# Optimization experiments

Hardware: AMD Instinct MI355X
Metric: run time of the kernel (lower is better)

Reference implementation:

```python
import jax, jax.numpy as jnp
import numpy as np

N = 50000; E = 800000; H = 4; C = 64; FEAT = 128; EDIM = 16; G = 256
NEG_SLOPE = 0.2; BN_EPS = 1e-5


def _gat_layer(x, src, dst, W, a_src, a_dst, bias, gamma, beta, alpha_edge=None):
    # GATConv (concat=True, PyG math), then BatchNorm1d (batch stats) + ReLU.
    h = (x @ W).reshape(N, H, C)                       # [N,H,C]
    alpha = (h * a_src).sum(-1)[src] + (h * a_dst).sum(-1)[dst]   # [Etot,H]
    if alpha_edge is not None:
        alpha = alpha + alpha_edge
    alpha = jax.nn.leaky_relu(alpha, NEG_SLOPE)
    amax = jax.ops.segment_max(alpha, dst, num_segments=N)        # edge softmax over dst
    ea = jnp.exp(alpha - amax[dst])
    denom = jax.ops.segment_sum(ea, dst, num_segments=N)
    coef = ea / (denom[dst] + 1e-16)
    out = jax.ops.segment_sum(coef[:, :, None] * h[src], dst, num_segments=N)
    out = out.reshape(N, H * C) + bias
    mu = out.mean(0)
    var = out.var(0)
    out = (out - mu) / jnp.sqrt(var + BN_EPS) * gamma + beta
    return jax.nn.relu(out)


def setup_inputs() -> dict:
    key = jax.random.key(0)
    ks = jax.random.split(key, 32)
    s = 0.05
    inp = {
        "x": jax.random.normal(ks[0], (N, FEAT), jnp.float32),
        "edge_index": jax.random.randint(ks[1], (2, E), 0, N),
        "edge_attr": jax.random.normal(ks[2], (E, EDIM), jnp.float32),
        "batch": jnp.sort(jax.random.randint(ks[3], (N,), 0, G)),
    }
    in_dims = [FEAT, H * C, H * C]
    for i in range(3):
        k = 4 + 7 * i
        inp[f"W{i}"] = jax.random.normal(ks[k], (in_dims[i], H * C), jnp.float32) * s
        inp[f"att_src{i}"] = jax.random.normal(ks[k + 1], (H, C), jnp.float32) * s
        inp[f"att_dst{i}"] = jax.random.normal(ks[k + 2], (H, C), jnp.float32) * s
        inp[f"bias{i}"] = jnp.zeros((H * C,), jnp.float32)
        inp[f"gamma{i}"] = jnp.ones((H * C,), jnp.float32)
        inp[f"beta{i}"] = jnp.zeros((H * C,), jnp.float32)
    inp["We0"] = jax.random.normal(ks[28], (EDIM, H * C), jnp.float32) * s
    inp["att_e0"] = jax.random.normal(ks[29], (H, C), jnp.float32) * s
    return inp


def reference(x, edge_index, edge_attr, batch,
              W0, att_src0, att_dst0, bias0, gamma0, beta0,
              W1, att_src1, att_dst1, bias1, gamma1, beta1,
              W2, att_src2, att_dst2, bias2, gamma2, beta2,
              We0, att_e0):
    # PyG GATConv adds self-loops; edge_attr for self-loops filled with mean.
    loops = jnp.arange(N)
    src = jnp.concatenate([edge_index[0], loops])
    dst = jnp.concatenate([edge_index[1], loops])
    ea_sl = jnp.concatenate([edge_attr, jnp.broadcast_to(edge_attr.mean(0), (N, EDIM))], 0)
    e = (ea_sl @ We0).reshape(E + N, H, C)
    alpha_e = (e * att_e0).sum(-1)                     # [Etot,H]
    x = _gat_layer(x, src, dst, W0, att_src0, att_dst0, bias0, gamma0, beta0, alpha_e)
    x = _gat_layer(x, src, dst, W1, att_src1, att_dst1, bias1, gamma1, beta1)
    x = _gat_layer(x, src, dst, W2, att_src2, att_dst2, bias2, gamma2, beta2)
    # global_mean_pool
    counts = jax.ops.segment_sum(jnp.ones((N,), x.dtype), batch, num_segments=G)
    sums = jax.ops.segment_sum(x, batch, num_segments=G)
    return sums / jnp.clip(counts, 1.0)[:, None]
```

## Files before the change

### kernel.cpp

```cpp
#include <hip/hip_runtime.h>
#include <math.h>

#define NN 50000
#define NE 800000
#define ET 850000
#define HCC 256
#define GG 256
#define CAP 64
#define NB 16

constexpr int RTILES = 782;

constexpr size_t NHC    = (size_t)NN * HCC;
constexpr size_t O_H    = 0;
constexpr size_t O_AGG  = O_H + NHC / 2;
constexpr size_t O_REC  = O_AGG + NHC / 2;
constexpr size_t O_BT0  = O_REC + (size_t)NN * CAP * 4;
constexpr size_t O_BT1  = O_BT0 + 16384;
constexpr size_t O_BT2  = O_BT1 + 32768;
constexpr size_t O_AS   = O_BT2 + 32768;
constexpr size_t O_AD   = O_AS + (size_t)NN * 4;
constexpr size_t O_M    = O_AD + (size_t)NN * 4;
constexpr size_t O_ZERO = O_M + 64;
constexpr size_t O_DEG  = O_ZERO;
constexpr size_t O_SLS  = O_DEG + NN;
constexpr size_t O_PART = O_SLS + 4;
constexpr size_t O_END  = O_PART + 3 * NB * 512;
constexpr size_t ZWORDS = O_END - O_ZERO;
constexpr int    ZBLK   = (int)((ZWORDS / 4 + 255) / 256);
constexpr int    XBLK   = (int)((size_t)NN * 128 / 2048);

typedef __attribute__((ext_vector_type(8))) short bf16x8;
typedef __attribute__((ext_vector_type(4))) float f32x4;

__device__ inline unsigned short f2bf(float f) {
    unsigned int u = __float_as_uint(f);
    unsigned int r = (u + 0x7fffu + ((u >> 16) & 1u)) >> 16;
    return (unsigned short)r;
}
__device__ inline float b2f(unsigned short u) {
    return __uint_as_float(((unsigned int)u) << 16);
}
__device__ inline float bflo(unsigned int u) { return __uint_as_float(u << 16); }
__device__ inline float bfhi(unsigned int u) { return __uint_as_float(u & 0xffff0000u); }

__global__ void prep_kernel(const float* __restrict__ W0, const float* __restrict__ W1,
                            const float* __restrict__ W2,
                            const float* __restrict__ We0, const float* __restrict__ att_e0,
                            unsigned short* __restrict__ Bt0,
                            unsigned short* __restrict__ Bt1,
                            unsigned short* __restrict__ Bt2,
                            float* __restrict__ M, float* __restrict__ zbase,
                            const float* __restrict__ x, unsigned short* __restrict__ xb) {
    int b = blockIdx.x;
    if (b >= 641 + ZBLK) {
        size_t i0 = ((size_t)(b - (641 + ZBLK)) * 256 + threadIdx.x) * 8;
        float4 f1 = *(const float4*)(x + i0);
        float4 f2 = *(const float4*)(x + i0 + 4);
        uint4 o;
        o.x = ((unsigned)f2bf(f1.y) << 16) | f2bf(f1.x);
        o.y = ((unsigned)f2bf(f1.w) << 16) | f2bf(f1.z);
        o.z = ((unsigned)f2bf(f2.y) << 16) | f2bf(f2.x);
        o.w = ((unsigned)f2bf(f2.w) << 16) | f2bf(f2.z);
        *(uint4*)(xb + i0) = o;
        return;
    }
    if (b >= 641) {
        size_t idx = ((size_t)(b - 641) * 256 + threadIdx.x) * 4;
        if (idx < ZWORDS)
            *(float4*)(zbase + idx) = make_float4(0.f, 0.f, 0.f, 0.f);
        return;
    }
    if (b == 640) {
        int t = threadIdx.x;
        if (t < 64) {
            int k = t >> 2, hh = t & 3;
            float s = 0.f;
            for (int c = 0; c < 64; ++c)
                s += We0[k * 256 + hh * 64 + c] * att_e0[hh * 64 + c];
            M[k * 4 + hh] = s;
        }
        return;
    }
    const float* W; unsigned short* Bt; int K, base;
    if (b < 128)      { W = W0; Bt = Bt0; K = 128; base = 0; }
    else if (b < 384) { W = W1; Bt = Bt1; K = 256; base = 128; }
    else              { W = W2; Bt = Bt2; K = 256; base = 384; }
    int idx = (b - base) * 256 + threadIdx.x;
    int n = idx & 255, k = idx >> 8;
    Bt[(size_t)n * K + k] = f2bf(W[(size_t)k * 256 + n]);
}

__global__ void csr_kernel(const int* __restrict__ srcA, const int* __restrict__ dstA,
                           const float* __restrict__ ea, const float* __restrict__ M,
                           int* __restrict__ deg, uint4* __restrict__ rec,
                           float* __restrict__ slsum) {
    int t0 = blockIdx.x * 2048 + threadIdx.x;
    float a0 = 0.f, a1 = 0.f, a2 = 0.f, a3 = 0.f;
    #pragma unroll
    for (int q = 0; q < 8; ++q) {
        int e = t0 + q * 256;
        if (e < ET) {
            bool real = (e < NE);
            int d = real ? dstA[e] : (e - NE);
            int s = real ? srcA[e] : (e - NE);
            int p = atomicAdd(&deg[d], 1);
            if (p > CAP - 1) p = CAP - 1;
            int slot = d * CAP + p;
            uint4 r;
            r.z = (unsigned)s;
            if (real) {
                r.w = 0u;
                const float4* pp = (const float4*)(ea + (size_t)e * 16);
                float4 va = pp[0], vb = pp[1], vc = pp[2], vd = pp[3];
                float v[16] = {va.x, va.y, va.z, va.w, vb.x, vb.y, vb.z, vb.w,
                               vc.x, vc.y, vc.z, vc.w, vd.x, vd.y, vd.z, vd.w};
                float o0 = 0.f, o1 = 0.f, o2 = 0.f, o3 = 0.f;
                #pragma unroll
                for (int k = 0; k < 16; ++k) {
                    float4 m4 = *(const float4*)(M + k * 4);
                    o0 = fmaf(v[k], m4.x, o0);
                    o1 = fmaf(v[k], m4.y, o1);
                    o2 = fmaf(v[k], m4.z, o2);
                    o3 = fmaf(v[k], m4.w, o3);
                }
                r.x = ((unsigned)f2bf(o1) << 16) | (unsigned)f2bf(o0);
                r.y = ((unsigned)f2bf(o3) << 16) | (unsigned)f2bf(o2);
                a0 += o0; a1 += o1; a2 += o2; a3 += o3;
            } else {
                r.x = 0u; r.y = 0u; r.w = 1u;
            }
            rec[slot] = r;
        }
    }
    #pragma unroll
    for (int off = 32; off; off >>= 1) {
        a0 += __shfl_xor(a0, off);
        a1 += __shfl_xor(a1, off);
        a2 += __shfl_xor(a2, off);
        a3 += __shfl_xor(a3, off);
    }
    __shared__ float part[4][4];
    int wave = threadIdx.x >> 6, lane = threadIdx.x & 63;
    if (lane == 0) {
        part[wave][0] = a0; part[wave][1] = a1;
        part[wave][2] = a2; part[wave][3] = a3;
    }
    __syncthreads();
    if (threadIdx.x < 4)
        atomicAdd(&slsum[threadIdx.x],
                  part[0][threadIdx.x] + part[1][threadIdx.x] +
                  part[2][threadIdx.x] + part[3][threadIdx.x]);
}

template <int K, bool NORM>
__global__ __launch_bounds__(512) void gemm2(const unsigned short* __restrict__ Ab,
                                             const unsigned short* __restrict__ Bt,
                                             const float* __restrict__ part,
                                             const float* __restrict__ gamma,
                                             const float* __restrict__ beta,
                                             const float* __restrict__ att_src,
                                             const float* __restrict__ att_dst,
                                             unsigned short* __restrict__ Hout,
                                             float* __restrict__ asA,
                                             float* __restrict__ adA, int M) {
    constexpr int KP  = K + 8;
    constexpr int NLD = K / 64;
    __shared__ unsigned short Bs[128][KP];
    __shared__ unsigned short As[2][64][KP];
    __shared__ float kvs[256], cvs[256];

    int tid = threadIdx.x;
    int wave = tid >> 6, lane = tid & 63;
    int quad = lane >> 4, l16 = lane & 15;
    int wr = wave >> 1, wc = wave & 1;

    int b = blockIdx.x;
    int cb = (b >> 3) & 1;
    int ts = ((b >> 4) << 3) | (b & 7);
    int np = (int)(gridDim.x >> 1);
    int colbase = cb * 128;
    int head = cb * 2 + wc;

    if (NORM) {
        if (tid < 256) {
            int ch = tid;
            float s = 0.f, s2 = 0.f;
            #pragma unroll
            for (int q = 0; q < NB; ++q) {
                s  += part[q * 512 + ch];
                s2 += part[q * 512 + 256 + ch];
            }
            const float invN = 1.0f / (float)NN;
            float mr = s * invN;
            float var = s2 * invN - mr * mr;
            float k = gamma[ch] * rsqrtf(var + 1e-5f);
            kvs[ch] = k;
            cvs[ch] = beta[ch] - mr * k;
        }
    }
    {
        constexpr int TOT = 128 * K;
        for (int idx = tid * 8; idx < TOT; idx += 4096) {
            int br = idx / K, bk = idx % K;
            uint4 v = *(const uint4*)(Bt + (size_t)(colbase + br) * K + bk);
            *(uint4*)&Bs[br][bk] = v;
        }
    }

    int srow = tid >> 3;
    const int scol0 = (tid & 7) * (K / 8);

    uint4 ldA_[NLD], ldB_[NLD];

    auto issue = [&](uint4 (&ld)[NLD], int t) {
        int r = t * 64 + srow;
        if (r < M) {
            const uint4* src = (const uint4*)(Ab + (size_t)r * K + scol0);
            #pragma unroll
            for (int q = 0; q < NLD; ++q) ld[q] = src[q];
        } else {
            #pragma unroll
            for (int q = 0; q < NLD; ++q) ld[q] = make_uint4(0u, 0u, 0u, 0u);
        }
    };
    auto commit = [&](uint4 (&ld)[NLD], int buf) {
        #pragma unroll
        for (int q = 0; q < NLD; ++q) {
            uint4 v = ld[q];
            if (NORM) {
                int ch = scol0 + q * 8;
                float u[8] = {bflo(v.x), bfhi(v.x), bflo(v.y), bfhi(v.y),
                              bflo(v.z), bfhi(v.z), bflo(v.w), bfhi(v.w)};
                #pragma unroll
                for (int j = 0; j < 8; ++j)
                    u[j] = fmaxf(fmaf(u[j], kvs[ch + j], cvs[ch + j]), 0.f);
                v.x = ((unsigned)f2bf(u[1]) << 16) | f2bf(u[0]);
                v.y = ((unsigned)f2bf(u[3]) << 16) | f2bf(u[2]);
                v.z = ((unsigned)f2bf(u[5]) << 16) | f2bf(u[4]);
                v.w = ((unsigned)f2bf(u[7]) << 16) | f2bf(u[6]);
            }
            *(uint4*)&As[buf][srow][scol0 + q * 8] = v;
        }
    };

    float asc[4], adc_[4];
    #pragma unroll
    for (int ni = 0; ni < 4; ++ni) {
        int c = colbase + wc * 64 + ni * 16 + l16;
        asc[ni]  = att_src[c];
        adc_[ni] = att_dst[c];
    }

    __syncthreads();

    auto tilestep = [&](uint4 (&ldCur)[NLD], uint4 (&ldNxt)[NLD], int buf, int t, int tn) {
        if (tn < RTILES) issue(ldNxt, tn);
        commit(ldCur, buf);
        __syncthreads();
        f32x4 acc[4] = {};
        #pragma unroll
        for (int k0 = 0; k0 < K; k0 += 32) {
            bf16x8 af, bfr[4];
            af = *(const bf16x8*)&As[buf][wr * 16 + l16][k0 + quad * 8];
            #pragma unroll
            for (int ni = 0; ni < 4; ++ni)
                bfr[ni] = *(const bf16x8*)&Bs[wc * 64 + ni * 16 + l16][k0 + quad * 8];
            #pragma unroll
            for (int ni = 0; ni < 4; ++ni)
                acc[ni] = __builtin_amdgcn_mfma_f32_16x16x32_bf16(
                    af, bfr[ni], acc[ni], 0, 0, 0);
        }
        int row0 = t * 64 + wr * 16;
        #pragma unroll
        for (int reg = 0; reg < 4; ++reg) {
            int r = row0 + quad * 4 + reg;
            if (r < M) {
                #pragma unroll
                for (int ni = 0; ni < 4; ++ni) {
                    int c = colbase + wc * 64 + ni * 16 + l16;
                    Hout[(size_t)r * HCC + c] = f2bf(acc[ni][reg]);
                }
            }
            float s1 = acc[0][reg] * asc[0] + acc[1][reg] * asc[1] +
                       acc[2][reg] * asc[2] + acc[3][reg] * asc[3];
            float d1 = acc[0][reg] * adc_[0] + acc[1][reg] * adc_[1] +
                       acc[2][reg] * adc_[2] + acc[3][reg] * adc_[3];
            #pragma unroll
            for (int off = 1; off < 16; off <<= 1) {
                s1 += __shfl_xor(s1, off);
                d1 += __shfl_xor(d1, off);
            }
            if (l16 == 0 && r < M) {
                asA[(size_t)r * 4 + head] = s1;
                adA[(size_t)r * 4 + head] = d1;
            }
        }
    };

    int t = ts;
    issue(ldA_, t);
    while (t < RTILES) {
        int t1 = t + np;
        tilestep(ldA_, ldB_, 0, t, t1);
        t = t1;
        if (t >= RTILES) break;
        int t2 = t + np;
        tilestep(ldB_, ldA_, 1, t, t2);
        t = t2;
    }
}

template <bool HAS_AE>
__global__ __launch_bounds__(512) void agg_kernel(const unsigned short* __restrict__ Hm,
                                                  const float* __restrict__ asA,
                                                  const float* __restrict__ adA,
                                                  const uint4* __restrict__ rec,
                                                  const int* __restrict__ degA,
                                                  const float* __restrict__ slsum,
                                                  unsigned short* __restrict__ outA,
                                                  float* __restrict__ part) {
    __shared__ float wlds[8][260];
    __shared__ float slds[2][8][256];
    int wave = threadIdx.x >> 6, lane = threadIdx.x & 63;
    int n = blockIdx.x * 8 + wave;
    int head = lane >> 4;
    int st = n * CAP;
    int d = degA[n];
    if (d > CAP) d = CAP;
    float4 ad4 = *(const float4*)(adA + (size_t)n * 4);

    float4 w4 = make_float4(0.f, 0.f, 0.f, 0.f);
    int ms = 0;
    if (lane < d) {
        uint4 r = rec[st + lane];
        ms = (int)r.z;
        float4 av = *(const float4*)(asA + (size_t)ms * 4);
        float4 t = make_float4(av.x + ad4.x, av.y + ad4.y, av.z + ad4.z, av.w + ad4.w);
        if (HAS_AE) {
            if (r.w) {
                const float inv = 1.0f / (float)NE;
                t.x += slsum[0] * inv; t.y += slsum[1] * inv;
                t.z += slsum[2] * inv; t.w += slsum[3] * inv;
            } else {
                t.x += bflo(r.x); t.y += bfhi(r.x);
                t.z += bflo(r.y); t.w += bfhi(r.y);
            }
        }
        t.x = (t.x > 0.f) ? t.x : 0.2f * t.x;
        t.y = (t.y > 0.f) ? t.y : 0.2f * t.y;
        t.z = (t.z > 0.f) ? t.z : 0.2f * t.z;
        t.w = (t.w > 0.f) ? t.w : 0.2f * t.w;
        w4.x = __expf(t.x);
        w4.y = __expf(t.y);
        w4.z = __expf(t.z);
        w4.w = __expf(t.w);
    }
    float4 Dv = w4;
    wlds[wave][0 * 65 + lane] = w4.x;
    wlds[wave][1 * 65 + lane] = w4.y;
    wlds[wave][2 * 65 + lane] = w4.z;
    wlds[wave][3 * 65 + lane] = w4.w;

    float4 acc = make_float4(0.f, 0.f, 0.f, 0.f);
    const unsigned short* hb = Hm + lane * 4;
    int cnt8 = (d + 7) & ~7;
    const float* wrow = &wlds[wave][head * 65];

    int sjA[8]; ushort4 hvA[8];
    #pragma unroll
    for (int q = 0; q < 8; ++q)
        sjA[q] = __builtin_amdgcn_readlane(ms, q);
    #pragma unroll
    for (int q = 0; q < 8; ++q)
        hvA[q] = *(const ushort4*)(hb + (size_t)sjA[q] * HCC);
    for (int jj = 0; jj < cnt8; jj += 8) {
        int nj = jj + 8;
        bool more = (nj < cnt8);
        ushort4 hvB[8];
        if (more) {
            int sjB[8];
            #pragma unroll
            for (int q = 0; q < 8; ++q)
                sjB[q] = __builtin_amdgcn_readlane(ms, nj + q);
            #pragma unroll
            for (int q = 0; q < 8; ++q)
                hvB[q] = *(const ushort4*)(hb + (size_t)sjB[q] * HCC);
        }
        float wq[8];
        #pragma unroll
        for (int q = 0; q < 8; ++q)
            wq[q] = wrow[jj + q];
        #pragma unroll
        for (int q = 0; q < 8; ++q) {
            acc.x = fmaf(wq[q], b2f(hvA[q].x), acc.x);
            acc.y = fmaf(wq[q], b2f(hvA[q].y), acc.y);
            acc.z = fmaf(wq[q], b2f(hvA[q].z), acc.z);
            acc.w = fmaf(wq[q], b2f(hvA[q].w), acc.w);
        }
        if (more) {
            #pragma unroll
            for (int q = 0; q < 8; ++q)
                hvA[q] = hvB[q];
        }
    }
    #pragma unroll
    for (int off = 32; off; off >>= 1) {
        Dv.x += __shfl_xor(Dv.x, off);
        Dv.y += __shfl_xor(Dv.y, off);
        Dv.z += __shfl_xor(Dv.z, off);
        Dv.w += __shfl_xor(Dv.w, off);
    }
    float D = (head & 2) ? ((head & 1) ? Dv.w : Dv.z) : ((head & 1) ? Dv.y : Dv.x);
    float inv = 1.0f / (D + 1e-16f);
    float4 o = make_float4(acc.x * inv, acc.y * inv, acc.z * inv, acc.w * inv);
    ushort4 ob = make_ushort4(f2bf(o.x), f2bf(o.y), f2bf(o.z), f2bf(o.w));
    *(ushort4*)(outA + (size_t)n * HCC + lane * 4) = ob;

    *(float4*)&slds[0][wave][lane * 4] = o;
    *(float4*)&slds[1][wave][lane * 4] =
        make_float4(o.x * o.x, o.y * o.y, o.z * o.z, o.w * o.w);
    __syncthreads();
    int t = threadIdx.x;
    if (t < 512) {
        int ch = t & 255, which = t >> 8;
        float s = 0.f;
        #pragma unroll
        for (int w = 0; w < 8; ++w)
            s += slds[which][w][ch];
        int bucket = blockIdx.x & (NB - 1);
        atomicAdd(&part[bucket * 512 + which * 256 + ch], s);
    }
}

__global__ void pool_kernel(const unsigned short* __restrict__ aggb,
                            const float* __restrict__ part,
                            const float* __restrict__ gamma, const float* __restrict__ beta,
                            const int* __restrict__ batch,
                            float* __restrict__ out) {
    int ch = threadIdx.x;
    int g = blockIdx.x;
    float s = 0.f, s2 = 0.f;
    #pragma unroll
    for (int b = 0; b < NB; ++b) {
        s  += part[b * 512 + ch];
        s2 += part[b * 512 + 256 + ch];
    }
    const float invN = 1.0f / (float)NN;
    float mr = s * invN;
    float var = s2 * invN - mr * mr;
    float k = gamma[ch] * rsqrtf(var + 1e-5f);
    float c = beta[ch] - mr * k;

    int lo = 0, hi = NN;
    while (lo < hi) { int mid = (lo + hi) >> 1; if (batch[mid] < g) lo = mid + 1; else hi = mid; }
    int start = lo;
    lo = start; hi = NN;
    while (lo < hi) { int mid = (lo + hi) >> 1; if (batch[mid] < g + 1) lo = mid + 1; else hi = mid; }
    int end = lo;

    float a0 = 0.f, a1 = 0.f, a2 = 0.f, a3 = 0.f;
    int n = start;
    for (; n + 3 < end; n += 4) {
        a0 += fmaxf(fmaf(b2f(aggb[(size_t)n * HCC + ch]), k, c), 0.f);
        a1 += fmaxf(fmaf(b2f(aggb[(size_t)(n + 1) * HCC + ch]), k, c), 0.f);
        a2 += fmaxf(fmaf(b2f(aggb[(size_t)(n + 2) * HCC + ch]), k, c), 0.f);
        a3 += fmaxf(fmaf(b2f(aggb[(size_t)(n + 3) * HCC + ch]), k, c), 0.f);
    }
    for (; n < end; ++n)
        a0 += fmaxf(fmaf(b2f(aggb[(size_t)n * HCC + ch]), k, c), 0.f);
    float tot = (a0 + a1) + (a2 + a3);
    out[(size_t)g * HCC + ch] = tot / fmaxf((float)(end - start), 1.0f);
}

extern "C" void kernel_launch(void* const* d_in, const int* in_sizes, int n_in,
                              void* d_out, int out_size, void* d_ws, size_t ws_size,
                              hipStream_t stream) {
    const float* x = (const float*)d_in[0];
    const int* edge_index = (const int*)d_in[1];
    const int* srcA = edge_index;
    const int* dstA = edge_index + NE;
    const float* edge_attr = (const float*)d_in[2];
    const int* batch = (const int*)d_in[3];
    const float* W[3]   = {(const float*)d_in[4],  (const float*)d_in[10], (const float*)d_in[16]};
    const float* asc[3] = {(const float*)d_in[5],  (const float*)d_in[11], (const float*)d_in[17]};
    const float* adc[3] = {(const float*)d_in[6],  (const float*)d_in[12], (const float*)d_in[18]};
    const float* gam[3] = {(const float*)d_in[8],  (const float*)d_in[14], (const float*)d_in[20]};
    const float* bet[3] = {(const float*)d_in[9],  (const float*)d_in[15], (const float*)d_in[21]};
    const float* We0 = (const float*)d_in[22];
    const float* att_e0 = (const float*)d_in[23];

    float* wsf = (float*)d_ws;
    unsigned short* hbuf = (unsigned short*)(wsf + O_H);
    unsigned short* aggb = (unsigned short*)(wsf + O_AGG);
    unsigned short* xb   = aggb;
    uint4* rec   = (uint4*)(wsf + O_REC);
    unsigned short* Bt0  = (unsigned short*)(wsf + O_BT0);
    unsigned short* Bt1  = (unsigned short*)(wsf + O_BT1);
    unsigned short* Bt2  = (unsigned short*)(wsf + O_BT2);
    float* asA   = wsf + O_AS;
    float* adA   = wsf + O_AD;
    float* Mb    = wsf + O_M;
    int*   deg   = (int*)(wsf + O_DEG);
    float* slsum = wsf + O_SLS;
    float* part  = wsf + O_PART;

    prep_kernel<<<641 + ZBLK + XBLK, 256, 0, stream>>>(W[0], W[1], W[2], We0, att_e0,
                                                       Bt0, Bt1, Bt2, Mb, wsf + O_ZERO,
                                                       x, xb);
    csr_kernel<<<(ET + 2047) / 2048, 256, 0, stream>>>(srcA, dstA, edge_attr, Mb,
                                                       deg, rec, slsum);

    gemm2<128, false><<<512, 512, 0, stream>>>(xb, Bt0, (const float*)0,
        (const float*)0, (const float*)0, asc[0], adc[0], hbuf, asA, adA, NN);
    agg_kernel<true><<<6250, 512, 0, stream>>>(hbuf, asA, adA, rec, deg, slsum,
        aggb, part + (size_t)0 * NB * 512);

    gemm2<256, true><<<256, 512, 0, stream>>>(aggb, Bt1, part + (size_t)0 * NB * 512,
        gam[0], bet[0], asc[1], adc[1], hbuf, asA, adA, NN);
    agg_kernel<false><<<6250, 512, 0, stream>>>(hbuf, asA, adA, rec, deg, slsum,
        aggb, part + (size_t)1 * NB * 512);

    gemm2<256, true><<<256, 512, 0, stream>>>(aggb, Bt2, part + (size_t)1 * NB * 512,
        gam[1], bet[1], asc[2], adc[2], hbuf, asA, adA, NN);
    agg_kernel<false><<<6250, 512, 0, stream>>>(hbuf, asA, adA, rec, deg, slsum,
        aggb, part + (size_t)2 * NB * 512);

    pool_kernel<<<GG, 256, 0, stream>>>(aggb, part + (size_t)2 * NB * 512,
                                        gam[2], bet[2], batch, (float*)d_out);
}
```

Before: 506.9 us.

## Load GEMM A fragments directly to registers, dropping LDS staging and double buffer

The node-feature GEMM kernel no longer stages A tiles through shared memory with a double-buffered pipeline and block barriers. Each wave now owns independent 16-row units and loads its A fragment directly from global memory into registers in MFMA layout, with BN+ReLU applied in registers. Launch bounds allow more blocks per CU, and layers 1-2 use twice as many blocks. This removes the LDS round-trip and per-tile barriers, but gives up cross-tile prefetch and relies on 50000 being divisible by 16, since row bounds checks are removed.

Result: slower. 744.4 us (+46.9%).

```diff
diff --git a/kernel.cpp b/kernel.cpp
--- a/kernel.cpp
+++ b/kernel.cpp
@@ -8,8 +8,6 @@
 #define GG 256
 #define CAP 64
 #define NB 16
-
-constexpr int RTILES = 782;
 
 constexpr size_t NHC    = (size_t)NN * HCC;
 constexpr size_t O_H    = 0;
@@ -154,33 +152,32 @@
 }
 
 template <int K, bool NORM>
-__global__ __launch_bounds__(512) void gemm2(const unsigned short* __restrict__ Ab,
-                                             const unsigned short* __restrict__ Bt,
-                                             const float* __restrict__ part,
-                                             const float* __restrict__ gamma,
-                                             const float* __restrict__ beta,
-                                             const float* __restrict__ att_src,
-                                             const float* __restrict__ att_dst,
-                                             unsigned short* __restrict__ Hout,
-                                             float* __restrict__ asA,
-                                             float* __restrict__ adA, int M) {
-    constexpr int KP  = K + 8;
-    constexpr int NLD = K / 64;
+__global__ __launch_bounds__(512, 4) void gemm3(const unsigned short* __restrict__ Ab,
+                                                const unsigned short* __restrict__ Bt,
+                                                const float* __restrict__ part,
+                                                const float* __restrict__ gamma,
+                                                const float* __restrict__ beta,
+                                                const float* __restrict__ att_src,
+                                                const float* __restrict__ att_dst,
+                                                unsigned short* __restrict__ Hout,
+                                                float* __restrict__ asA,
+                                                float* __restrict__ adA) {
+    constexpr int KP = K + 8;
+    constexpr int NS = K / 32;
     __shared__ unsigned short Bs[128][KP];
-    __shared__ unsigned short As[2][64][KP];
     __shared__ float kvs[256], cvs[256];
 
     int tid = threadIdx.x;
     int wave = tid >> 6, lane = tid & 63;
     int quad = lane >> 4, l16 = lane & 15;
-    int wr = wave >> 1, wc = wave & 1;
+    int slot = wave >> 1, wc = wave & 1;
 
     int b = blockIdx.x;
     int cb = (b >> 3) & 1;
-    int ts = ((b >> 4) << 3) | (b & 7);
-    int np = (int)(gridDim.x >> 1);
+    int pair = ((b >> 4) << 3) | (b & 7);
     int colbase = cb * 128;
     int head = cb * 2 + wc;
+    int unit = pair * 4 + slot;
 
     if (NORM) {
         if (tid < 256) {
@@ -208,79 +205,64 @@
         }
     }
 
-    int srow = tid >> 3;
-    const int scol0 = (tid & 7) * (K / 8);
-
-    uint4 ldA_[NLD], ldB_[NLD];
-
-    auto issue = [&](uint4 (&ld)[NLD], int t) {
-        int r = t * 64 + srow;
-        if (r < M) {
-            const uint4* src = (const uint4*)(Ab + (size_t)r * K + scol0);
-            #pragma unroll
-            for (int q = 0; q < NLD; ++q) ld[q] = src[q];
-        } else {
-            #pragma unroll
-            for (int q = 0; q < NLD; ++q) ld[q] = make_uint4(0u, 0u, 0u, 0u);
-        }
-    };
-    auto commit = [&](uint4 (&ld)[NLD], int buf) {
+    float asc[4], adc_[4];
+    #pragma unroll
+    for (int ni = 0; ni < 4; ++ni) {
+        int c = colbase + wc * 64 + ni * 16 + l16;
+        asc[ni]  = att_src[c];
+        adc_[ni] = att_dst[c];
+    }
+
+    __syncthreads();
+
+    for (int t = unit; t < 3125; t += 1024) {
+        int row = t * 16 + l16;
+        const unsigned short* ap = Ab + (size_t)row * K + quad * 8;
+        uint4 al[NS];
         #pragma unroll
-        for (int q = 0; q < NLD; ++q) {
-            uint4 v = ld[q];
+        for (int s = 0; s < NS; ++s)
+            al[s] = *(const uint4*)(ap + s * 32);
+
+        f32x4 acc[4] = {};
+        #pragma unroll
+        for (int s = 0; s < NS; ++s) {
+            union { uint4 u; bf16x8 h; } cvt;
             if (NORM) {
-                int ch = scol0 + q * 8;
+                uint4 v = al[s];
+                int ch = s * 32 + quad * 8;
                 float u[8] = {bflo(v.x), bfhi(v.x), bflo(v.y), bfhi(v.y),
                               bflo(v.z), bfhi(v.z), bflo(v.w), bfhi(v.w)};
                 #pragma unroll
                 for (int j = 0; j < 8; ++j)
                     u[j] = fmaxf(fmaf(u[j], kvs[ch + j], cvs[ch + j]), 0.f);
-                v.x = ((unsigned)f2bf(u[1]) << 16) | f2bf(u[0]);
-                v.y = ((unsigned)f2bf(u[3]) << 16) | f2bf(u[2]);
-                v.z = ((unsigned)f2bf(u[5]) << 16) | f2bf(u[4]);
-                v.w = ((unsigned)f2bf(u[7]) << 16) | f2bf(u[6]);
-            }
-            *(uint4*)&As[buf][srow][scol0 + q * 8] = v;
-        }
-    };
-
-    float asc[4], adc_[4];
-    #pragma unroll
-    for (int ni = 0; ni < 4; ++ni) {
-        int c = colbase + wc * 64 + ni * 16 + l16;
-        asc[ni]  = att_src[c];
-        adc_[ni] = att_dst[c];
-    }
-
-    __syncthreads();
-
-    auto tilestep = [&](uint4 (&ldCur)[NLD], uint4 (&ldNxt)[NLD], int buf, int t, int tn) {
-        if (tn < RTILES) issue(ldNxt, tn);
-        commit(ldCur, buf);
-        __syncthreads();
-        f32x4 acc[4] = {};
-        #pragma unroll
-        for (int k0 = 0; k0 < K; k0 += 32) {
-            bf16x8 af, bfr[4];
-            af = *(const bf16x8*)&As[buf][wr * 16 + l16][k0 + quad * 8];
+                uint4 w;
+                w.x = ((unsigned)f2bf(u[1]) << 16) | f2bf(u[0]);
+                w.y = ((unsigned)f2bf(u[3]) << 16) | f2bf(u[2]);
+                w.z = ((unsigned)f2bf(u[5]) << 16) | f2bf(u[4]);
+                w.w = ((unsigned)f2bf(u[7]) << 16) | f2bf(u[6]);
+                cvt.u = w;
+            } else {
+                cvt.u = al[s];
+            }
+            bf16x8 af = cvt.h;
+            bf16x8 bfr[4];
             #pragma unroll
             for (int ni = 0; ni < 4; ++ni)
-                bfr[ni] = *(const bf16x8*)&Bs[wc * 64 + ni * 16 + l16][k0 + quad * 8];
+                bfr[ni] = *(const bf16x8*)&Bs[wc * 64 + ni * 16 + l16][s * 32 + quad * 8];
             #pragma unroll
             for (int ni = 0; ni < 4; ++ni)
                 acc[ni] = __builtin_amdgcn_mfma_f32_16x16x32_bf16(
                     af, bfr[ni], acc[ni], 0, 0, 0);
         }
-        int row0 = t * 64 + wr * 16;
+
+        int row0 = t * 16;
         #pragma unroll
         for (int reg = 0; reg < 4; ++reg) {
             int r = row0 + quad * 4 + reg;
-            if (r < M) {
-                #pragma unroll
-                for (int ni = 0; ni < 4; ++ni) {
-                    int c = colbase + wc * 64 + ni * 16 + l16;
-                    Hout[(size_t)r * HCC + c] = f2bf(acc[ni][reg]);
-                }
+            #pragma unroll
+            for (int ni = 0; ni < 4; ++ni) {
+                int c = colbase + wc * 64 + ni * 16 + l16;
+                Hout[(size_t)r * HCC + c] = f2bf(acc[ni][reg]);
             }
             float s1 = acc[0][reg] * asc[0] + acc[1][reg] * asc[1] +
                        acc[2][reg] * asc[2] + acc[3][reg] * asc[3];
@@ -291,23 +273,11 @@
                 s1 += __shfl_xor(s1, off);
                 d1 += __shfl_xor(d1, off);
             }
-            if (l16 == 0 && r < M) {
+            if (l16 == 0) {
                 asA[(size_t)r * 4 + head] = s1;
                 adA[(size_t)r * 4 + head] = d1;
             }
         }
-    };
-
-    int t = ts;
-    issue(ldA_, t);
-    while (t < RTILES) {
-        int t1 = t + np;
-        tilestep(ldA_, ldB_, 0, t, t1);
-        t = t1;
-        if (t >= RTILES) break;
-        int t2 = t + np;
-        tilestep(ldB_, ldA_, 1, t, t2);
-        t = t2;
     }
 }
 
@@ -511,18 +481,18 @@
     csr_kernel<<<(ET + 2047) / 2048, 256, 0, stream>>>(srcA, dstA, edge_attr, Mb,
                                                        deg, rec, slsum);
 
-    gemm2<128, false><<<512, 512, 0, stream>>>(xb, Bt0, (const float*)0,
-        (const float*)0, (const float*)0, asc[0], adc[0], hbuf, asA, adA, NN);
+    gemm3<128, false><<<512, 512, 0, stream>>>(xb, Bt0, (const float*)0,
+        (const float*)0, (const float*)0, asc[0], adc[0], hbuf, asA, adA);
     agg_kernel<true><<<6250, 512, 0, stream>>>(hbuf, asA, adA, rec, deg, slsum,
         aggb, part + (size_t)0 * NB * 512);
 
-    gemm2<256, true><<<256, 512, 0, stream>>>(aggb, Bt1, part + (size_t)0 * NB * 512,
-        gam[0], bet[0], asc[1], adc[1], hbuf, asA, adA, NN);
+    gemm3<256, true><<<512, 512, 0, stream>>>(aggb, Bt1, part + (size_t)0 * NB * 512,
+        gam[0], bet[0], asc[1], adc[1], hbuf, asA, adA);
     agg_kernel<false><<<6250, 512, 0, stream>>>(hbuf, asA, adA, rec, deg, slsum,
         aggb, part + (size_t)1 * NB * 512);
 
-    gemm2<256, true><<<256, 512, 0, stream>>>(aggb, Bt2, part + (size_t)1 * NB * 512,
-        gam[1], bet[1], asc[2], adc[2], hbuf, asA, adA, NN);
+    gemm3<256, true><<<512, 512, 0, stream>>>(aggb, Bt2, part + (size_t)1 * NB * 512,
+        gam[1], bet[1], asc[2], adc[2], hbuf, asA, adA);
     agg_kernel<false><<<6250, 512, 0, stream>>>(hbuf, asA, adA, rec, deg, slsum,
         aggb, part + (size_t)2 * NB * 512);
 
```

## Fuse layer-0 GEMM with CSR build and deepen aggregation gather prefetch

Applied to the files above, without the earlier changes.

Merges the CSR/edge-record construction and the first-layer GEMM into a single launch, with separate block ranges, so the two independent stages run concurrently and one launch gap disappears. The aggregation kernel now uses 256-thread blocks with 4 nodes each, doubling the block count. Its neighbor gather is restructured into two 8-wide register buffers, so two batches of loads are in flight instead of one. These changes raise register pressure in the aggregation kernel, and the fused kernel's CSR blocks share the GPU with GEMM blocks.

New measurement: 520.0 us. +2.6%, slower.

```diff
diff --git a/kernel.cpp b/kernel.cpp
--- a/kernel.cpp
+++ b/kernel.cpp
@@ -10,6 +10,8 @@
 #define NB 16
 
 constexpr int RTILES = 782;
+constexpr int G0B    = 512;
+constexpr int CSRB   = 416;
 
 constexpr size_t NHC    = (size_t)NN * HCC;
 constexpr size_t O_H    = 0;
@@ -91,66 +93,197 @@
     Bt[(size_t)n * K + k] = f2bf(W[(size_t)k * 256 + n]);
 }
 
-__global__ void csr_kernel(const int* __restrict__ srcA, const int* __restrict__ dstA,
-                           const float* __restrict__ ea, const float* __restrict__ M,
-                           int* __restrict__ deg, uint4* __restrict__ rec,
-                           float* __restrict__ slsum) {
-    int t0 = blockIdx.x * 2048 + threadIdx.x;
-    float a0 = 0.f, a1 = 0.f, a2 = 0.f, a3 = 0.f;
+__global__ __launch_bounds__(512) void g0csr(const unsigned short* __restrict__ Ab,
+                                             const unsigned short* __restrict__ Bt,
+                                             const float* __restrict__ att_src,
+                                             const float* __restrict__ att_dst,
+                                             unsigned short* __restrict__ Hout,
+                                             float* __restrict__ asA,
+                                             float* __restrict__ adA,
+                                             const int* __restrict__ srcA,
+                                             const int* __restrict__ dstA,
+                                             const float* __restrict__ ea,
+                                             const float* __restrict__ Mm,
+                                             int* __restrict__ deg,
+                                             uint4* __restrict__ rec,
+                                             float* __restrict__ slsum) {
+    constexpr int K   = 128;
+    constexpr int KP  = K + 8;
+    constexpr int NLD = K / 64;
+    __shared__ unsigned short Bs[128][KP];
+    __shared__ unsigned short As[2][64][KP];
+    __shared__ float prt[8][4];
+
+    int tid = threadIdx.x;
+    int wave = tid >> 6, lane = tid & 63;
+
+    if (blockIdx.x >= G0B) {
+        int t0 = (int)(blockIdx.x - G0B) * 2048 + tid;
+        float a0 = 0.f, a1 = 0.f, a2 = 0.f, a3 = 0.f;
+        #pragma unroll
+        for (int q = 0; q < 4; ++q) {
+            int e = t0 + q * 512;
+            if (e < ET) {
+                bool real = (e < NE);
+                int d = real ? dstA[e] : (e - NE);
+                int s = real ? srcA[e] : (e - NE);
+                int p = atomicAdd(&deg[d], 1);
+                if (p > CAP - 1) p = CAP - 1;
+                int slot = d * CAP + p;
+                uint4 r;
+                r.z = (unsigned)s;
+                if (real) {
+                    r.w = 0u;
+                    const float4* pp = (const float4*)(ea + (size_t)e * 16);
+                    float4 va = pp[0], vb = pp[1], vc = pp[2], vd = pp[3];
+                    float v[16] = {va.x, va.y, va.z, va.w, vb.x, vb.y, vb.z, vb.w,
+                                   vc.x, vc.y, vc.z, vc.w, vd.x, vd.y, vd.z, vd.w};
+                    float o0 = 0.f, o1 = 0.f, o2 = 0.f, o3 = 0.f;
+                    #pragma unroll
+                    for (int k = 0; k < 16; ++k) {
+                        float4 m4 = *(const float4*)(Mm + k * 4);
+                        o0 = fmaf(v[k], m4.x, o0);
+                        o1 = fmaf(v[k], m4.y, o1);
+                        o2 = fmaf(v[k], m4.z, o2);
+                        o3 = fmaf(v[k], m4.w, o3);
+                    }
+                    r.x = ((unsigned)f2bf(o1) << 16) | (unsigned)f2bf(o0);
+                    r.y = ((unsigned)f2bf(o3) << 16) | (unsigned)f2bf(o2);
+                    a0 += o0; a1 += o1; a2 += o2; a3 += o3;
+                } else {
+                    r.x = 0u; r.y = 0u; r.w = 1u;
+                }
+                rec[slot] = r;
+            }
+        }
+        #pragma unroll
+        for (int off = 32; off; off >>= 1) {
+            a0 += __shfl_xor(a0, off);
+            a1 += __shfl_xor(a1, off);
+            a2 += __shfl_xor(a2, off);
+            a3 += __shfl_xor(a3, off);
+        }
+        if (lane == 0) {
+            prt[wave][0] = a0; prt[wave][1] = a1;
+            prt[wave][2] = a2; prt[wave][3] = a3;
+        }
+        __syncthreads();
+        if (tid < 4) {
+            float s = 0.f;
+            #pragma unroll
+            for (int w = 0; w < 8; ++w) s += prt[w][tid];
+            atomicAdd(&slsum[tid], s);
+        }
+        return;
+    }
+
+    int quad = lane >> 4, l16 = lane & 15;
+    int wr = wave >> 1, wc = wave & 1;
+
+    int b = blockIdx.x;
+    int cb = (b >> 3) & 1;
+    int ts = ((b >> 4) << 3) | (b & 7);
+    const int np = G0B >> 1;
+    int colbase = cb * 128;
+    int head = cb * 2 + wc;
+
+    {
+        constexpr int TOT = 128 * K;
+        for (int idx = tid * 8; idx < TOT; idx += 4096) {
+            int br = idx / K, bk = idx % K;
+            uint4 v = *(const uint4*)(Bt + (size_t)(colbase + br) * K + bk);
+            *(uint4*)&Bs[br][bk] = v;
+        }
+    }
+
+    int srow = tid >> 3;
+    const int scol0 = (tid & 7) * (K / 8);
+
+    uint4 ldA_[NLD], ldB_[NLD];
+
+    auto issue = [&](uint4 (&ld)[NLD], int t) {
+        int r = t * 64 + srow;
+        if (r < NN) {
+            const uint4* src = (const uint4*)(Ab + (size_t)r * K + scol0);
+            #pragma unroll
+            for (int q = 0; q < NLD; ++q) ld[q] = src[q];
+        } else {
+            #pragma unroll
+            for (int q = 0; q < NLD; ++q) ld[q] = make_uint4(0u, 0u, 0u, 0u);
+        }
+    };
+    auto commit = [&](uint4 (&ld)[NLD], int buf) {
+        #pragma unroll
+        for (int q = 0; q < NLD; ++q)
+            *(uint4*)&As[buf][srow][scol0 + q * 8] = ld[q];
+    };
+
+    float asc[4], adc_[4];
     #pragma unroll
-    for (int q = 0; q < 8; ++q) {
-        int e = t0 + q * 256;
-        if (e < ET) {
-            bool real = (e < NE);
-            int d = real ? dstA[e] : (e - NE);
-            int s = real ? srcA[e] : (e - NE);
-            int p = atomicAdd(&deg[d], 1);
-            if (p > CAP - 1) p = CAP - 1;
-            int slot = d * CAP + p;
-            uint4 r;
-            r.z = (unsigned)s;
-            if (real) {
-                r.w = 0u;
-                const float4* pp = (const float4*)(ea + (size_t)e * 16);
-                float4 va = pp[0], vb = pp[1], vc = pp[2], vd = pp[3];
-                float v[16] = {va.x, va.y, va.z, va.w, vb.x, vb.y, vb.z, vb.w,
-                               vc.x, vc.y, vc.z, vc.w, vd.x, vd.y, vd.z, vd.w};
-                float o0 = 0.f, o1 = 0.f, o2 = 0.f, o3 = 0.f;
+    for (int ni = 0; ni < 4; ++ni) {
+        int c = colbase + wc * 64 + ni * 16 + l16;
+        asc[ni]  = att_src[c];
+        adc_[ni] = att_dst[c];
+    }
+
+    __syncthreads();
+
+    auto tilestep = [&](uint4 (&ldCur)[NLD], uint4 (&ldNxt)[NLD], int buf, int t, int tn) {
+        if (tn < RTILES) issue(ldNxt, tn);
+        commit(ldCur, buf);
+        __syncthreads();
+
+        f32x4 acc[4] = {};
+        #pragma unroll
+        for (int k0 = 0; k0 < K; k0 += 32) {
+            bf16x8 af, bfr[4];
+            af = *(const bf16x8*)&As[buf][wr * 16 + l16][k0 + quad * 8];
+            #pragma unroll
+            for (int ni = 0; ni < 4; ++ni)
+                bfr[ni] = *(const bf16x8*)&Bs[wc * 64 + ni * 16 + l16][k0 + quad * 8];
+            #pragma unroll
+            for (int ni = 0; ni < 4; ++ni)
+                acc[ni] = __builtin_amdgcn_mfma_f32_16x16x32_bf16(
+                    af, bfr[ni], acc[ni], 0, 0, 0);
+        }
+        int row0 = t * 64 + wr * 16;
+        #pragma unroll
+        for (int reg = 0; reg < 4; ++reg) {
+            int r = row0 + quad * 4 + reg;
+            if (r < NN) {
                 #pragma unroll
-                for (int k = 0; k < 16; ++k) {
-                    float4 m4 = *(const float4*)(M + k * 4);
-                    o0 = fmaf(v[k], m4.x, o0);
-                    o1 = fmaf(v[k], m4.y, o1);
-                    o2 = fmaf(v[k], m4.z, o2);
-                    o3 = fmaf(v[k], m4.w, o3);
+                for (int ni = 0; ni < 4; ++ni) {
+                    int c = colbase + wc * 64 + ni * 16 + l16;
+                    Hout[(size_t)r * HCC + c] = f2bf(acc[ni][reg]);
                 }
-                r.x = ((unsigned)f2bf(o1) << 16) | (unsigned)f2bf(o0);
-                r.y = ((unsigned)f2bf(o3) << 16) | (unsigned)f2bf(o2);
-                a0 += o0; a1 += o1; a2 += o2; a3 += o3;
-            } else {
-                r.x = 0u; r.y = 0u; r.w = 1u;
-            }
-            rec[slot] = r;
-        }
-    }
-    #pragma unroll
-    for (int off = 32; off; off >>= 1) {
-        a0 += __shfl_xor(a0, off);
-        a1 += __shfl_xor(a1, off);
-        a2 += __shfl_xor(a2, off);
-        a3 += __shfl_xor(a3, off);
-    }
-    __shared__ float part[4][4];
-    int wave = threadIdx.x >> 6, lane = threadIdx.x & 63;
-    if (lane == 0) {
-        part[wave][0] = a0; part[wave][1] = a1;
-        part[wave][2] = a2; part[wave][3] = a3;
-    }
-    __syncthreads();
-    if (threadIdx.x < 4)
-        atomicAdd(&slsum[threadIdx.x],
-                  part[0][threadIdx.x] + part[1][threadIdx.x] +
-                  part[2][threadIdx.x] + part[3][threadIdx.x]);
+            }
+            float s1 = acc[0][reg] * asc[0] + acc[1][reg] * asc[1] +
+                       acc[2][reg] * asc[2] + acc[3][reg] * asc[3];
+            float d1 = acc[0][reg] * adc_[0] + acc[1][reg] * adc_[1] +
+                       acc[2][reg] * adc_[2] + acc[3][reg] * adc_[3];
+            #pragma unroll
+            for (int off = 1; off < 16; off <<= 1) {
+                s1 += __shfl_xor(s1, off);
+                d1 += __shfl_xor(d1, off);
+            }
+            if (l16 == 0 && r < NN) {
+                asA[(size_t)r * 4 + head] = s1;
+                adA[(size_t)r * 4 + head] = d1;
+            }
+        }
+    };
+
+    int t = ts;
+    issue(ldA_, t);
+    while (t < RTILES) {
+        int t1 = t + np;
+        tilestep(ldA_, ldB_, 0, t, t1);
+        t = t1;
+        if (t >= RTILES) break;
+        int t2 = t + np;
+        tilestep(ldB_, ldA_, 1, t, t2);
+        t = t2;
+    }
 }
 
 template <int K, bool NORM>
@@ -312,7 +445,7 @@
 }
 
 template <bool HAS_AE>
-__global__ __launch_bounds__(512) void agg_kernel(const unsigned short* __restrict__ Hm,
+__global__ __launch_bounds__(256) void agg_kernel(const unsigned short* __restrict__ Hm,
                                                   const float* __restrict__ asA,
                                                   const float* __restrict__ adA,
                                                   const uint4* __restrict__ rec,
@@ -320,10 +453,10 @@
                                                   const float* __restrict__ slsum,
                                                   unsigned short* __restrict__ outA,
                                                   float* __restrict__ part) {
-    __shared__ float wlds[8][260];
-    __shared__ float slds[2][8][256];
+    __shared__ float wlds[4][260];
+    __shared__ float slds[2][4][256];
     int wave = threadIdx.x >> 6, lane = threadIdx.x & 63;
-    int n = blockIdx.x * 8 + wave;
+    int n = blockIdx.x * 4 + wave;
     int head = lane >> 4;
     int st = n * CAP;
     int d = degA[n];
@@ -367,41 +500,64 @@
     int cnt8 = (d + 7) & ~7;
     const float* wrow = &wlds[wave][head * 65];
 
-    int sjA[8]; ushort4 hvA[8];
+    int sj0[8], sj1[8];
+    ushort4 hv0[8], hv1[8];
     #pragma unroll
     for (int q = 0; q < 8; ++q)
-        sjA[q] = __builtin_amdgcn_readlane(ms, q);
+        sj0[q] = __builtin_amdgcn_readlane(ms, q);
     #pragma unroll
     for (int q = 0; q < 8; ++q)
-        hvA[q] = *(const ushort4*)(hb + (size_t)sjA[q] * HCC);
-    for (int jj = 0; jj < cnt8; jj += 8) {
-        int nj = jj + 8;
-        bool more = (nj < cnt8);
-        ushort4 hvB[8];
-        if (more) {
-            int sjB[8];
+        hv0[q] = *(const ushort4*)(hb + (size_t)sj0[q] * HCC);
+    if (cnt8 > 8) {
+        #pragma unroll
+        for (int q = 0; q < 8; ++q)
+            sj1[q] = __builtin_amdgcn_readlane(ms, 8 + q);
+        #pragma unroll
+        for (int q = 0; q < 8; ++q)
+            hv1[q] = *(const ushort4*)(hb + (size_t)sj1[q] * HCC);
+    }
+    for (int jj = 0; jj < cnt8; jj += 16) {
+        {
+            float wq[8];
             #pragma unroll
             for (int q = 0; q < 8; ++q)
-                sjB[q] = __builtin_amdgcn_readlane(ms, nj + q);
+                wq[q] = wrow[jj + q];
+            #pragma unroll
+            for (int q = 0; q < 8; ++q) {
+                acc.x = fmaf(wq[q], b2f(hv0[q].x), acc.x);
+                acc.y = fmaf(wq[q], b2f(hv0[q].y), acc.y);
+                acc.z = fmaf(wq[q], b2f(hv0[q].z), acc.z);
+                acc.w = fmaf(wq[q], b2f(hv0[q].w), acc.w);
+            }
+            if (jj + 16 < cnt8) {
+                #pragma unroll
+                for (int q = 0; q < 8; ++q)
+                    sj0[q] = __builtin_amdgcn_readlane(ms, jj + 16 + q);
+                #pragma unroll
+                for (int q = 0; q < 8; ++q)
+                    hv0[q] = *(const ushort4*)(hb + (size_t)sj0[q] * HCC);
+            }
+        }
+        if (jj + 8 < cnt8) {
+            float wq[8];
             #pragma unroll
             for (int q = 0; q < 8; ++q)
-                hvB[q] = *(const ushort4*)(hb + (size_t)sjB[q] * HCC);
-        }
-        float wq[8];
-        #pragma unroll
-        for (int q = 0; q < 8; ++q)
-            wq[q] = wrow[jj + q];
-        #pragma unroll
-        for (int q = 0; q < 8; ++q) {
-            acc.x = fmaf(wq[q], b2f(hvA[q].x), acc.x);
-            acc.y = fmaf(wq[q], b2f(hvA[q].y), acc.y);
-            acc.z = fmaf(wq[q], b2f(hvA[q].z), acc.z);
-            acc.w = fmaf(wq[q], b2f(hvA[q].w), acc.w);
-        }
-        if (more) {
-            #pragma unroll
-            for (int q = 0; q < 8; ++q)
-                hvA[q] = hvB[q];
+                wq[q] = wrow[jj + 8 + q];
+            #pragma unroll
+            for (int q = 0; q < 8; ++q) {
+                acc.x = fmaf(wq[q], b2f(hv1[q].x), acc.x);
+                acc.y = fmaf(wq[q], b2f(hv1[q].y), acc.y);
+                acc.z = fmaf(wq[q], b2f(hv1[q].z), acc.z);
+                acc.w = fmaf(wq[q], b2f(hv1[q].w), acc.w);
+            }
+            if (jj + 24 < cnt8) {
+                #pragma unroll
+                for (int q = 0; q < 8; ++q)
+                    sj1[q] = __builtin_amdgcn_readlane(ms, jj + 24 + q);
+                #pragma unroll
+                for (int q = 0; q < 8; ++q)
+                    hv1[q] = *(const ushort4*)(hb + (size_t)sj1[q] * HCC);
+            }
         }
     }
     #pragma unroll
@@ -421,15 +577,17 @@
     *(float4*)&slds[1][wave][lane * 4] =
         make_float4(o.x * o.x, o.y * o.y, o.z * o.z, o.w * o.w);
     __syncthreads();
-    int t = threadIdx.x;
-    if (t < 512) {
-        int ch = t & 255, which = t >> 8;
-        float s = 0.f;
-        #pragma unroll
-        for (int w = 0; w < 8; ++w)
-            s += slds[which][w][ch];
+    {
+        int ch = threadIdx.x;
+        float s0 = 0.f, s1 = 0.f;
+        #pragma unroll
+        for (int w = 0; w < 4; ++w) {
+            s0 += slds[0][w][ch];
+            s1 += slds[1][w][ch];
+        }
         int bucket = blockIdx.x & (NB - 1);
-        atomicAdd(&part[bucket * 512 + which * 256 + ch], s);
+        atomicAdd(&part[bucket * 512 + ch], s0);
+        atomicAdd(&part[bucket * 512 + 256 + ch], s1);
     }
 }
 
@@ -508,22 +666,20 @@
     prep_kernel<<<641 + ZBLK + XBLK, 256, 0, stream>>>(W[0], W[1], W[2], We0, att_e0,
                                                        Bt0, Bt1, Bt2, Mb, wsf + O_ZERO,
                                                        x, xb);
-    csr_kernel<<<(ET + 2047) / 2048, 256, 0, stream>>>(srcA, dstA, edge_attr, Mb,
-                                                       deg, rec, slsum);
-
-    gemm2<128, false><<<512, 512, 0, stream>>>(xb, Bt0, (const float*)0,
-        (const float*)0, (const float*)0, asc[0], adc[0], hbuf, asA, adA, NN);
-    agg_kernel<true><<<6250, 512, 0, stream>>>(hbuf, asA, adA, rec, deg, slsum,
+
+    g0csr<<<G0B + CSRB, 512, 0, stream>>>(xb, Bt0, asc[0], adc[0], hbuf, asA, adA,
+                                          srcA, dstA, edge_attr, Mb, deg, rec, slsum);
+    agg_kernel<true><<<12500, 256, 0, stream>>>(hbuf, asA, adA, rec, deg, slsum,
         aggb, part + (size_t)0 * NB * 512);
 
     gemm2<256, true><<<256, 512, 0, stream>>>(aggb, Bt1, part + (size_t)0 * NB * 512,
         gam[0], bet[0], asc[1], adc[1], hbuf, asA, adA, NN);
-    agg_kernel<false><<<6250, 512, 0, stream>>>(hbuf, asA, adA, rec, deg, slsum,
+    agg_kernel<false><<<12500, 256, 0, stream>>>(hbuf, asA, adA, rec, deg, slsum,
         aggb, part + (size_t)1 * NB * 512);
 
     gemm2<256, true><<<256, 512, 0, stream>>>(aggb, Bt2, part + (size_t)1 * NB * 512,
         gam[1], bet[1], asc[2], adc[2], hbuf, asA, adA, NN);
-    agg_kernel<false><<<6250, 512, 0, stream>>>(hbuf, asA, adA, rec, deg, slsum,
+    agg_kernel<false><<<12500, 256, 0, stream>>>(hbuf, asA, adA, rec, deg, slsum,
         aggb, part + (size_t)2 * NB * 512);
 
     pool_kernel<<<GG, 256, 0, stream>>>(aggb, part + (size_t)2 * NB * 512,
```
